# Optimization experiments

Hardware: AMD Instinct MI355X
Metric: run time of the kernel (lower is better)

## Reference

```python
import jax, jax.numpy as jnp
import numpy as np


def setup_inputs() -> dict:
    key = jax.random.key(0)
    k0, k1, k2, k3, k4 = jax.random.split(key, 5)
    B, S, H, I, E = 4, 2048, 1024, 3584, 8
    scale = 0.02
    return {
        "hidden_states": jax.random.normal(k0, (B, S, H), jnp.float32),
        "gate_w": jax.random.normal(k1, (E, H), jnp.float32) * scale,
        "Wg": jax.random.normal(k2, (E, I, H), jnp.float32) * scale,
        "Wu": jax.random.normal(k3, (E, I, H), jnp.float32) * scale,
        "Wd": jax.random.normal(k4, (E, H, I), jnp.float32) * scale,
        "top_k": 2,
    }


def reference(hidden_states, gate_w, Wg, Wu, Wd, top_k):
    B, S, H = hidden_states.shape
    E = gate_w.shape[0]
    x = hidden_states.reshape(-1, H)  # [N, H]

    # Router: softmax in float32 (matches torch dtype=torch.float), then top-k + renorm.
    router_logits = x @ gate_w.T  # [N, E]
    routing_probs = jax.nn.softmax(router_logits.astype(jnp.float32), axis=-1)
    top_w, sel = jax.lax.top_k(routing_probs, top_k)  # [N, K]
    top_w = top_w / jnp.sum(top_w, axis=-1, keepdims=True)
    top_w = top_w.astype(x.dtype)

    # Combined per-token weight for each expert: sum of top-k weights routed to it.
    # comb[n, e] = sum_k top_w[n, k] * (sel[n, k] == e)
    comb = jnp.einsum("nk,nke->ne", top_w, jax.nn.one_hot(sel, E, dtype=x.dtype))

    out = jnp.zeros_like(x)
    for e in range(E):  # fixed small loop over experts (structurally distinct weights)
        h = jax.nn.silu(x @ Wg[e].T) * (x @ Wu[e].T)  # [N, I] SwiGLU
        out = out + (h @ Wd[e].T) * comb[:, e:e + 1]
    return out.reshape(B, S, H), router_logits
```

## Files before the change

### kernel.cpp

```cpp
#include <hip/hip_runtime.h>
#include <hip/hip_bf16.h>

#define N_TOK 8192
#define H_DIM 1024
#define I_DIM 3584
#define N_EXP 8
#define N_PAIR (N_TOK * 2)

#define BM 256
#define BN 128
#define BK 32
#define MAX_TILES 72

#define NPAN1 (I_DIM / BN)
#define NPAN2 (H_DIM / BN)
#define NWG1  (MAX_TILES * NPAN1)
#define NWG2  (MAX_TILES * NPAN2)

typedef short bf16x8 __attribute__((ext_vector_type(8)));
typedef float f32x4 __attribute__((ext_vector_type(4)));

#define WS_CNT      0
#define WS_FILL     64
#define WS_OFF      128
#define WS_NTILES   192
#define WS_TILETAB  256
#define WS_SEL      2048
#define WS_WGT      (WS_SEL    + 2 * N_TOK * 4)
#define WS_PTOK     (WS_WGT    + 2 * N_TOK * 4)
#define WS_PW       (WS_PTOK   + N_PAIR * 4)
#define WS_XBF      (WS_PW     + N_PAIR * 4)
#define WS_HBUF     (WS_XBF    + (size_t)N_TOK * H_DIM * 2)
#define WBF_ELEMS   ((size_t)N_EXP * I_DIM * H_DIM)
#define WS_WGBF     (WS_HBUF + (size_t)N_PAIR * I_DIM * 2)
#define WS_WUBF     (WS_WGBF + WBF_ELEMS * 2)
#define WS_END      (WS_WUBF + WBF_ELEMS * 2)

__device__ __forceinline__ unsigned short f2bf(float f) {
  unsigned int u = __float_as_uint(f);
  unsigned int r = (u + 0x7fffu + ((u >> 16) & 1u)) >> 16;
  return (unsigned short)r;
}

__device__ __forceinline__ uint4 pack8(float4 a, float4 b) {
  uint4 r;
  r.x = (unsigned)f2bf(a.x) | ((unsigned)f2bf(a.y) << 16);
  r.y = (unsigned)f2bf(a.z) | ((unsigned)f2bf(a.w) << 16);
  r.z = (unsigned)f2bf(b.x) | ((unsigned)f2bf(b.y) << 16);
  r.w = (unsigned)f2bf(b.z) | ((unsigned)f2bf(b.w) << 16);
  return r;
}

__device__ __forceinline__ void gll16(const ushort* g, ushort* l) {
  __builtin_amdgcn_global_load_lds(
      (const __attribute__((address_space(1))) unsigned int*)g,
      (__attribute__((address_space(3))) unsigned int*)l, 16, 0, 0);
}

__global__ __launch_bounds__(64) void k_router(
    const float* __restrict__ x, const float* __restrict__ gw,
    float* __restrict__ logits, int* __restrict__ sel,
    float* __restrict__ wgt, int* __restrict__ cnt,
    ushort* __restrict__ xbf)
{
  const int n = blockIdx.x;
  const int lane = threadIdx.x;
  const float4* xr = (const float4*)(x + (size_t)n * H_DIM + lane * 16);
  float4 x0 = xr[0], x1 = xr[1], x2 = xr[2], x3 = xr[3];

  uint4* xo = (uint4*)(xbf + (size_t)n * H_DIM + lane * 16);
  xo[0] = pack8(x0, x1);
  xo[1] = pack8(x2, x3);

  float l[N_EXP];
#pragma unroll
  for (int e = 0; e < N_EXP; ++e) {
    const float4* wr = (const float4*)(gw + e * H_DIM + lane * 16);
    float4 w0 = wr[0], w1 = wr[1], w2 = wr[2], w3 = wr[3];
    float p = x0.x * w0.x + x0.y * w0.y + x0.z * w0.z + x0.w * w0.w
            + x1.x * w1.x + x1.y * w1.y + x1.z * w1.z + x1.w * w1.w
            + x2.x * w2.x + x2.y * w2.y + x2.z * w2.z + x2.w * w2.w
            + x3.x * w3.x + x3.y * w3.y + x3.z * w3.z + x3.w * w3.w;
#pragma unroll
    for (int o = 32; o >= 1; o >>= 1) p += __shfl_xor(p, o, 64);
    l[e] = p;
  }
  float m = l[0];
#pragma unroll
  for (int e = 1; e < N_EXP; ++e) m = fmaxf(m, l[e]);
  float pr[N_EXP]; float den = 0.f;
#pragma unroll
  for (int e = 0; e < N_EXP; ++e) { pr[e] = expf(l[e] - m); den += pr[e]; }
#pragma unroll
  for (int e = 0; e < N_EXP; ++e) pr[e] /= den;
  int i0 = 0; float p0 = pr[0];
#pragma unroll
  for (int e = 1; e < N_EXP; ++e) { if (pr[e] > p0) { p0 = pr[e]; i0 = e; } }
  int i1 = -1; float p1 = -1.f;
#pragma unroll
  for (int e = 0; e < N_EXP; ++e) { if (e != i0 && pr[e] > p1) { p1 = pr[e]; i1 = e; } }
  float rs = 1.f / (p0 + p1);
  if (lane == 0) {
    float* lo = logits + (size_t)n * N_EXP;
#pragma unroll
    for (int e = 0; e < N_EXP; ++e) lo[e] = l[e];
    sel[2 * n] = i0; sel[2 * n + 1] = i1;
    wgt[2 * n] = p0 * rs; wgt[2 * n + 1] = p1 * rs;
    atomicAdd(&cnt[i0], 1);
    atomicAdd(&cnt[i1], 1);
  }
}

__global__ void k_prefix(const int* __restrict__ cnt, int* __restrict__ off,
                         int* __restrict__ ntiles, int* __restrict__ tab)
{
  if (threadIdx.x != 0 || blockIdx.x != 0) return;
  int acc = 0, nt = 0;
  for (int e = 0; e < N_EXP; ++e) {
    off[e] = acc;
    int c = cnt[e];
    for (int r = 0; r < c; r += BM) {
      tab[nt * 3 + 0] = e;
      tab[nt * 3 + 1] = acc + r;
      tab[nt * 3 + 2] = (c - r < BM) ? (c - r) : BM;
      nt++;
    }
    acc += c;
  }
  off[N_EXP] = acc;
  *ntiles = nt;
}

__global__ __launch_bounds__(256) void k_scatter(
    const int* __restrict__ sel, const float* __restrict__ wgt,
    const int* __restrict__ off, int* __restrict__ fill,
    int* __restrict__ ptok, float* __restrict__ pw)
{
  int n = blockIdx.x * 256 + threadIdx.x;
  if (n >= N_TOK) return;
#pragma unroll
  for (int k = 0; k < 2; ++k) {
    int e = sel[2 * n + k];
    int pos = atomicAdd(&fill[e], 1);
    int row = off[e] + pos;
    ptok[row] = n;
    pw[row] = wgt[2 * n + k];
  }
}

__global__ __launch_bounds__(256) void k_cvtw(const float* __restrict__ src,
                                              ushort* __restrict__ dst)
{
  size_t i = (size_t)blockIdx.x * 256 + threadIdx.x;
  const float4* s = (const float4*)(src + i * 8);
  float4 a = s[0], b = s[1];
  ((uint4*)dst)[i] = pack8(a, b);
}


__global__ __launch_bounds__(512) void k_mlp1b(
    const ushort* __restrict__ Wg, const ushort* __restrict__ Wu,
    const ushort* __restrict__ xbf, const int* __restrict__ ptok,
    const int* __restrict__ ntiles, const int* __restrict__ tab,
    ushort* __restrict__ hbuf)
{
  __shared__ ushort sA[2][BM * BK];
  __shared__ ushort sG[2][BN * BK];
  __shared__ ushort sU[2][BN * BK];
  __shared__ int stok[BM];

  const int orig = blockIdx.x;
  const int lin = (orig & 7) * (NWG1 >> 3) + (orig >> 3);
  const int tile = lin / NPAN1;
  const int i0 = (lin % NPAN1) * BN;

  if (tile >= *ntiles) return;
  const int e = tab[tile * 3 + 0];
  const int row0 = tab[tile * 3 + 1];
  const int nrows = tab[tile * 3 + 2];
  const int t = threadIdx.x;

  if (t < BM) {
    int tt = t < nrows ? t : (nrows - 1);
    stok[t] = ptok[row0 + tt];
  }
  __syncthreads();

  const int ak = (t & 3) * 8;
  const int ar = t >> 2;
  const ushort* ga0 = xbf + (size_t)stok[ar] * H_DIM + ak;
  const ushort* ga1 = xbf + (size_t)stok[128 + ar] * H_DIM + ak;

  const ushort* gg0 = Wg + (size_t)e * I_DIM * H_DIM + (size_t)(i0 + ar) * H_DIM + ak;
  const ushort* gu0 = Wu + (size_t)e * I_DIM * H_DIM + (size_t)(i0 + ar) * H_DIM + ak;

  const int lane = t & 63, wid = t >> 6;
  const int wm = wid >> 1, wn = wid & 1;
  const int fr = lane & 15, fq = lane >> 4;

  f32x4 ag[4][4], au[4][4];
#pragma unroll
  for (int m = 0; m < 4; ++m)
#pragma unroll
    for (int n = 0; n < 4; ++n) { ag[m][n] = (f32x4){0,0,0,0}; au[m][n] = (f32x4){0,0,0,0}; }

#define STAGE1(b, kt) do {                      \
    gll16(ga0 + (kt), &sA[b][t * 8]);           \
    gll16(ga1 + (kt), &sA[b][(512 + t) * 8]);   \
    gll16(gg0 + (kt), &sG[b][t * 8]);           \
    gll16(gu0 + (kt), &sU[b][t * 8]);           \
  } while (0)

#define COMPUTE1(b) do {                                                     \
    bf16x8 a[4], bg[4], bu[4];                                               \
    _Pragma("unroll")                                                        \
    for (int m = 0; m < 4; ++m)                                              \
      a[m] = *(const bf16x8*)(&sA[b][(wm * 64 + m * 16 + fr) * BK + fq * 8]);\
    _Pragma("unroll")                                                        \
    for (int n = 0; n < 4; ++n) {                                            \
      bg[n] = *(const bf16x8*)(&sG[b][(wn * 64 + n * 16 + fr) * BK + fq * 8]);\
      bu[n] = *(const bf16x8*)(&sU[b][(wn * 64 + n * 16 + fr) * BK + fq * 8]);\
    }                                                                        \
    _Pragma("unroll")                                                        \
    for (int m = 0; m < 4; ++m)                                              \
      _Pragma("unroll")                                                      \
      for (int n = 0; n < 4; ++n) {                                          \
        ag[m][n] = __builtin_amdgcn_mfma_f32_16x16x32_bf16(a[m], bg[n], ag[m][n], 0, 0, 0); \
        au[m][n] = __builtin_amdgcn_mfma_f32_16x16x32_bf16(a[m], bu[n], au[m][n], 0, 0, 0); \
      }                                                                      \
  } while (0)

  const int NK = H_DIM / BK;
  STAGE1(0, 0);
  __syncthreads();
  for (int ki = 0; ki < NK - 1; ++ki) {
    const int cur = ki & 1;
    STAGE1(cur ^ 1, (ki + 1) * BK);
    COMPUTE1(cur);
    __syncthreads();
  }
  COMPUTE1((NK - 1) & 1);
#undef STAGE1
#undef COMPUTE1

#pragma unroll
  for (int m = 0; m < 4; ++m) {
    const int rb = wm * 64 + m * 16 + fq * 4;
#pragma unroll
    for (int n = 0; n < 4; ++n) {
      const int col = i0 + wn * 64 + n * 16 + fr;
#pragma unroll
      for (int r = 0; r < 4; ++r) {
        const int row = rb + r;
        if (row < nrows) {
          float g = ag[m][n][r], u = au[m][n][r];
          float hv = (g / (1.f + __expf(-g))) * u;
          hbuf[(size_t)(row0 + row) * I_DIM + col] = f2bf(hv);
        }
      }
    }
  }
}

__global__ __launch_bounds__(512) void k_mlp2b(
    const ushort* __restrict__ Wd, const ushort* __restrict__ hbuf,
    const int* __restrict__ ptok, const float* __restrict__ pw,
    const int* __restrict__ ntiles, const int* __restrict__ tab,
    float* __restrict__ out)
{
  __shared__ ushort sA[2][BM * BK];
  __shared__ ushort sB[2][BN * BK];
  __shared__ int stok[BM];
  __shared__ float sw[BM];

  const int orig = blockIdx.x;
  const int lin = (orig & 7) * (NWG2 >> 3) + (orig >> 3);
  const int tile = lin / NPAN2;
  const int j0 = (lin % NPAN2) * BN;

  if (tile >= *ntiles) return;
  const int e = tab[tile * 3 + 0];
  const int row0 = tab[tile * 3 + 1];
  const int nrows = tab[tile * 3 + 2];
  const int t = threadIdx.x;

  if (t < BM) {
    int tt = t < nrows ? t : (nrows - 1);
    stok[t] = ptok[row0 + tt];
    sw[t] = pw[row0 + tt];
  }
  __syncthreads();

  const int ak = (t & 3) * 8;
  const int ar = t >> 2;
  int arow0 = row0 + ar;        if (arow0 > N_PAIR - 1) arow0 = N_PAIR - 1;
  int arow1 = row0 + 128 + ar;  if (arow1 > N_PAIR - 1) arow1 = N_PAIR - 1;
  const ushort* ga0 = hbuf + (size_t)arow0 * I_DIM + ak;
  const ushort* ga1 = hbuf + (size_t)arow1 * I_DIM + ak;

  const ushort* gb0 = Wd + (size_t)e * H_DIM * I_DIM + (size_t)(j0 + ar) * I_DIM + ak;

  const int lane = t & 63, wid = t >> 6;
  const int wm = wid >> 1, wn = wid & 1;
  const int fr = lane & 15, fq = lane >> 4;

  f32x4 ac[4][4];
#pragma unroll
  for (int m = 0; m < 4; ++m)
#pragma unroll
    for (int n = 0; n < 4; ++n) ac[m][n] = (f32x4){0,0,0,0};

#define STAGE2(b, kt) do {                      \
    gll16(ga0 + (kt), &sA[b][t * 8]);           \
    gll16(ga1 + (kt), &sA[b][(512 + t) * 8]);   \
    gll16(gb0 + (kt), &sB[b][t * 8]);           \
  } while (0)

#define COMPUTE2(b) do {                                                     \
    bf16x8 a[4], bb[4];                                                      \
    _Pragma("unroll")                                                        \
    for (int m = 0; m < 4; ++m)                                              \
      a[m] = *(const bf16x8*)(&sA[b][(wm * 64 + m * 16 + fr) * BK + fq * 8]);\
    _Pragma("unroll")                                                        \
    for (int n = 0; n < 4; ++n)                                              \
      bb[n] = *(const bf16x8*)(&sB[b][(wn * 64 + n * 16 + fr) * BK + fq * 8]);\
    _Pragma("unroll")                                                        \
    for (int m = 0; m < 4; ++m)                                              \
      _Pragma("unroll")                                                      \
      for (int n = 0; n < 4; ++n)                                            \
        ac[m][n] = __builtin_amdgcn_mfma_f32_16x16x32_bf16(a[m], bb[n], ac[m][n], 0, 0, 0); \
  } while (0)

  const int NK = I_DIM / BK;
  STAGE2(0, 0);
  __syncthreads();
  for (int ki = 0; ki < NK - 1; ++ki) {
    const int cur = ki & 1;
    STAGE2(cur ^ 1, (ki + 1) * BK);
    COMPUTE2(cur);
    __syncthreads();
  }
  COMPUTE2((NK - 1) & 1);
#undef STAGE2
#undef COMPUTE2

#pragma unroll
  for (int m = 0; m < 4; ++m) {
    const int rb = wm * 64 + m * 16 + fq * 4;
#pragma unroll
    for (int n = 0; n < 4; ++n) {
      const int col = j0 + wn * 64 + n * 16 + fr;
#pragma unroll
      for (int r = 0; r < 4; ++r) {
        const int row = rb + r;
        if (row < nrows) {
          float v = ac[m][n][r] * sw[row];
          atomicAdd(&out[(size_t)stok[row] * H_DIM + col], v);
        }
      }
    }
  }
}


#define FBM 128

__global__ __launch_bounds__(256) void k_mlp1(
    const float* __restrict__ Wg, const float* __restrict__ Wu,
    const ushort* __restrict__ xbf, const int* __restrict__ ptok,
    const int* __restrict__ ntiles, const int* __restrict__ tab,
    ushort* __restrict__ hbuf)
{
  __shared__ ushort sA[FBM * BK];
  __shared__ ushort sG[BN * BK];
  __shared__ ushort sU[BN * BK];
  __shared__ int stok[FBM];

  const int tile = blockIdx.x;
  if (tile >= *ntiles) return;
  const int e = tab[tile * 3 + 0];
  const int row0 = tab[tile * 3 + 1] + (blockIdx.z ? FBM : 0);
  int nrows = tab[tile * 3 + 2] - (blockIdx.z ? FBM : 0);
  if (nrows <= 0) return;
  if (nrows > FBM) nrows = FBM;
  const int i0 = blockIdx.y * BN;
  const int t = threadIdx.x;

  if (t < FBM) {
    int tt = t < nrows ? t : (nrows - 1);
    stok[t] = ptok[row0 + tt];
  }
  __syncthreads();

  const int ak = (t & 3) * 8;
  const ushort* ga0 = xbf + (size_t)stok[t >> 2] * H_DIM + ak;
  const ushort* ga1 = xbf + (size_t)stok[64 + (t >> 2)] * H_DIM + ak;
  ushort* la0 = sA + (size_t)t * 8;
  ushort* la1 = sA + (size_t)(256 + t) * 8;

  const int wr = t >> 1, wcb = (t & 1) * 16;
  const float* gwg = Wg + (size_t)e * I_DIM * H_DIM + (size_t)(i0 + wr) * H_DIM + wcb;
  const float* gwu = Wu + (size_t)e * I_DIM * H_DIM + (size_t)(i0 + wr) * H_DIM + wcb;
  ushort* lwg = sG + wr * BK + wcb;
  ushort* lwu = sU + wr * BK + wcb;

  const int lane = t & 63, wid = t >> 6;
  const int wm = wid >> 1, wn = wid & 1;
  const int fr = lane & 15, fq = lane >> 4;

  f32x4 ag[4][4], au[4][4];
#pragma unroll
  for (int m = 0; m < 4; ++m)
#pragma unroll
    for (int n = 0; n < 4; ++n) { ag[m][n] = (f32x4){0,0,0,0}; au[m][n] = (f32x4){0,0,0,0}; }

  for (int kt = 0; kt < H_DIM; kt += BK) {
    gll16(ga0 + kt, la0);
    gll16(ga1 + kt, la1);

    const float4* pg = (const float4*)(gwg + kt);
    const float4* pu = (const float4*)(gwu + kt);
    float4 g0 = pg[0], g1 = pg[1], g2 = pg[2], g3 = pg[3];
    float4 u0 = pu[0], u1 = pu[1], u2 = pu[2], u3 = pu[3];
    ((uint4*)lwg)[0] = pack8(g0, g1);
    ((uint4*)lwg)[1] = pack8(g2, g3);
    ((uint4*)lwu)[0] = pack8(u0, u1);
    ((uint4*)lwu)[1] = pack8(u2, u3);
    __syncthreads();

    bf16x8 a[4], bg[4], bu[4];
#pragma unroll
    for (int m = 0; m < 4; ++m)
      a[m] = *(const bf16x8*)(sA + (wm * 64 + m * 16 + fr) * BK + fq * 8);
#pragma unroll
    for (int n = 0; n < 4; ++n) {
      bg[n] = *(const bf16x8*)(sG + (wn * 64 + n * 16 + fr) * BK + fq * 8);
      bu[n] = *(const bf16x8*)(sU + (wn * 64 + n * 16 + fr) * BK + fq * 8);
    }
#pragma unroll
    for (int m = 0; m < 4; ++m)
#pragma unroll
      for (int n = 0; n < 4; ++n) {
        ag[m][n] = __builtin_amdgcn_mfma_f32_16x16x32_bf16(a[m], bg[n], ag[m][n], 0, 0, 0);
        au[m][n] = __builtin_amdgcn_mfma_f32_16x16x32_bf16(a[m], bu[n], au[m][n], 0, 0, 0);
      }
    __syncthreads();
  }

#pragma unroll
  for (int m = 0; m < 4; ++m) {
    const int rb = wm * 64 + m * 16 + fq * 4;
#pragma unroll
    for (int n = 0; n < 4; ++n) {
      const int col = i0 + wn * 64 + n * 16 + fr;
#pragma unroll
      for (int r = 0; r < 4; ++r) {
        const int row = rb + r;
        if (row < nrows) {
          float g = ag[m][n][r], u = au[m][n][r];
          float hv = (g / (1.f + __expf(-g))) * u;
          hbuf[(size_t)(row0 + row) * I_DIM + col] = f2bf(hv);
        }
      }
    }
  }
}

__global__ __launch_bounds__(256) void k_mlp2(
    const float* __restrict__ Wd, const ushort* __restrict__ hbuf,
    const int* __restrict__ ptok, const float* __restrict__ pw,
    const int* __restrict__ ntiles, const int* __restrict__ tab,
    float* __restrict__ out)
{
  __shared__ ushort sA[FBM * BK];
  __shared__ ushort sB[BN * BK];
  __shared__ int stok[FBM];
  __shared__ float sw[FBM];

  const int tile = blockIdx.x;
  if (tile >= *ntiles) return;
  const int e = tab[tile * 3 + 0];
  const int row0 = tab[tile * 3 + 1] + (blockIdx.z ? FBM : 0);
  int nrows = tab[tile * 3 + 2] - (blockIdx.z ? FBM : 0);
  if (nrows <= 0) return;
  if (nrows > FBM) nrows = FBM;
  const int j0 = blockIdx.y * BN;
  const int t = threadIdx.x;

  if (t < FBM) {
    int tt = t < nrows ? t : (nrows - 1);
    stok[t] = ptok[row0 + tt];
    sw[t] = pw[row0 + tt];
  }
  __syncthreads();

  const int ak = (t & 3) * 8;
  int arow0 = row0 + (t >> 2);       if (arow0 > N_PAIR - 1) arow0 = N_PAIR - 1;
  int arow1 = row0 + 64 + (t >> 2);  if (arow1 > N_PAIR - 1) arow1 = N_PAIR - 1;
  const ushort* ga0 = hbuf + (size_t)arow0 * I_DIM + ak;
  const ushort* ga1 = hbuf + (size_t)arow1 * I_DIM + ak;
  ushort* la0 = sA + (size_t)t * 8;
  ushort* la1 = sA + (size_t)(256 + t) * 8;

  const int wr = t >> 1, wcb = (t & 1) * 16;
  const float* gb = Wd + (size_t)e * H_DIM * I_DIM + (size_t)(j0 + wr) * I_DIM + wcb;
  ushort* lb = sB + wr * BK + wcb;

  const int lane = t & 63, wid = t >> 6;
  const int wm = wid >> 1, wn = wid & 1;
  const int fr = lane & 15, fq = lane >> 4;

  f32x4 ac[4][4];
#pragma unroll
  for (int m = 0; m < 4; ++m)
#pragma unroll
    for (int n = 0; n < 4; ++n) ac[m][n] = (f32x4){0,0,0,0};

  for (int kt = 0; kt < I_DIM; kt += BK) {
    gll16(ga0 + kt, la0);
    gll16(ga1 + kt, la1);

    const float4* pb = (const float4*)(gb + kt);
    float4 b0 = pb[0], b1 = pb[1], b2 = pb[2], b3 = pb[3];
    ((uint4*)lb)[0] = pack8(b0, b1);
    ((uint4*)lb)[1] = pack8(b2, b3);
    __syncthreads();

    bf16x8 a[4], bb[4];
#pragma unroll
    for (int m = 0; m < 4; ++m)
      a[m] = *(const bf16x8*)(sA + (wm * 64 + m * 16 + fr) * BK + fq * 8);
#pragma unroll
    for (int n = 0; n < 4; ++n)
      bb[n] = *(const bf16x8*)(sB + (wn * 64 + n * 16 + fr) * BK + fq * 8);
#pragma unroll
    for (int m = 0; m < 4; ++m)
#pragma unroll
      for (int n = 0; n < 4; ++n)
        ac[m][n] = __builtin_amdgcn_mfma_f32_16x16x32_bf16(a[m], bb[n], ac[m][n], 0, 0, 0);
    __syncthreads();
  }

#pragma unroll
  for (int m = 0; m < 4; ++m) {
    const int rb = wm * 64 + m * 16 + fq * 4;
#pragma unroll
    for (int n = 0; n < 4; ++n) {
      const int col = j0 + wn * 64 + n * 16 + fr;
#pragma unroll
      for (int r = 0; r < 4; ++r) {
        const int row = rb + r;
        if (row < nrows) {
          float v = ac[m][n][r] * sw[row];
          atomicAdd(&out[(size_t)stok[row] * H_DIM + col], v);
        }
      }
    }
  }
}

extern "C" void kernel_launch(void* const* d_in, const int* in_sizes, int n_in,
                              void* d_out, int out_size, void* d_ws, size_t ws_size,
                              hipStream_t stream)
{
  const float* x  = (const float*)d_in[0];
  const float* gw = (const float*)d_in[1];
  const float* Wg = (const float*)d_in[2];
  const float* Wu = (const float*)d_in[3];
  const float* Wd = (const float*)d_in[4];

  float* out    = (float*)d_out;
  float* logits = out + (size_t)N_TOK * H_DIM;

  char* ws = (char*)d_ws;
  int*    cnt    = (int*)(ws + WS_CNT);
  int*    fill   = (int*)(ws + WS_FILL);
  int*    off    = (int*)(ws + WS_OFF);
  int*    ntiles = (int*)(ws + WS_NTILES);
  int*    tab    = (int*)(ws + WS_TILETAB);
  int*    sel    = (int*)(ws + WS_SEL);
  float*  wgt    = (float*)(ws + WS_WGT);
  int*    ptok   = (int*)(ws + WS_PTOK);
  float*  pw     = (float*)(ws + WS_PW);
  ushort* xbf    = (ushort*)(ws + WS_XBF);
  ushort* hbuf   = (ushort*)(ws + WS_HBUF);
  ushort* wgbf   = (ushort*)(ws + WS_WGBF);
  ushort* wubf   = (ushort*)(ws + WS_WUBF);
  ushort* wdbf   = wgbf;

  const bool fast = (ws_size >= WS_END);

  hipMemsetAsync(d_out, 0, (size_t)N_TOK * H_DIM * sizeof(float), stream);
  hipMemsetAsync(ws, 0, 128, stream);

  k_router<<<N_TOK, 64, 0, stream>>>(x, gw, logits, sel, wgt, cnt, xbf);
  k_prefix<<<1, 64, 0, stream>>>(cnt, off, ntiles, tab);
  k_scatter<<<N_TOK / 256, 256, 0, stream>>>(sel, wgt, off, fill, ptok, pw);

  const int cvtblocks = (int)(WBF_ELEMS / 8 / 256);

  if (fast) {
    k_cvtw<<<cvtblocks, 256, 0, stream>>>(Wg, wgbf);
    k_cvtw<<<cvtblocks, 256, 0, stream>>>(Wu, wubf);
    k_mlp1b<<<NWG1, 512, 0, stream>>>(wgbf, wubf, xbf, ptok, ntiles, tab, hbuf);
    k_cvtw<<<cvtblocks, 256, 0, stream>>>(Wd, wdbf);
    k_mlp2b<<<NWG2, 512, 0, stream>>>(wdbf, hbuf, ptok, pw, ntiles, tab, out);
  } else {
    dim3 gA(MAX_TILES, I_DIM / BN, 2);
    dim3 gB(MAX_TILES, H_DIM / BN, 2);
    k_mlp1<<<gA, 256, 0, stream>>>(Wg, Wu, xbf, ptok, ntiles, tab, hbuf);
    k_mlp2<<<gB, 256, 0, stream>>>(Wd, hbuf, ptok, pw, ntiles, tab, out);
  }
}
```

Baseline: 985.1 us.

## Overlap global-to-LDS staging with MFMA via manual waitcnt and barriers

Restructures both expert GEMM main loops into a two-stage prefetch pipeline. The next-next tile is issued right after compute, and the loop waits with partial vmcnt counts and raw s_barrier instead of __syncthreads. The goal is to keep global loads in flight while the MFMAs run, instead of draining all memory traffic at each barrier. The hard-coded vmcnt values assume a fixed number of load instructions per STAGE macro (4 and 3), so a different code generation could cause races.

```diff
diff --git a/kernel.cpp b/kernel.cpp
--- a/kernel.cpp
+++ b/kernel.cpp
@@ -19,6 +19,8 @@
 
 typedef short bf16x8 __attribute__((ext_vector_type(8)));
 typedef float f32x4 __attribute__((ext_vector_type(4)));
+
+#define CFENCE() asm volatile("" ::: "memory")
 
 #define WS_CNT      0
 #define WS_FILL     64
@@ -232,14 +234,33 @@
 
   const int NK = H_DIM / BK;
   STAGE1(0, 0);
-  __syncthreads();
-  for (int ki = 0; ki < NK - 1; ++ki) {
+  CFENCE();
+  STAGE1(1, BK);
+#pragma unroll 2
+  for (int ki = 0; ki < NK - 2; ++ki) {
     const int cur = ki & 1;
-    STAGE1(cur ^ 1, (ki + 1) * BK);
+    asm volatile("s_waitcnt vmcnt(4)" ::: "memory");
+    __builtin_amdgcn_s_barrier();
+    CFENCE();
+    __builtin_amdgcn_sched_barrier(0);
     COMPUTE1(cur);
-    __syncthreads();
-  }
-  COMPUTE1((NK - 1) & 1);
+    asm volatile("s_waitcnt lgkmcnt(0)" ::: "memory");
+    __builtin_amdgcn_sched_barrier(0);
+    __builtin_amdgcn_s_barrier();
+    CFENCE();
+    STAGE1(cur, (ki + 2) * BK);
+  }
+  asm volatile("s_waitcnt vmcnt(4)" ::: "memory");
+  __builtin_amdgcn_s_barrier();
+  CFENCE();
+  __builtin_amdgcn_sched_barrier(0);
+  COMPUTE1(0);
+  CFENCE();
+  asm volatile("s_waitcnt vmcnt(0) lgkmcnt(0)" ::: "memory");
+  __builtin_amdgcn_s_barrier();
+  CFENCE();
+  __builtin_amdgcn_sched_barrier(0);
+  COMPUTE1(1);
 #undef STAGE1
 #undef COMPUTE1
 
@@ -333,14 +354,33 @@
 
   const int NK = I_DIM / BK;
   STAGE2(0, 0);
-  __syncthreads();
-  for (int ki = 0; ki < NK - 1; ++ki) {
+  CFENCE();
+  STAGE2(1, BK);
+#pragma unroll 2
+  for (int ki = 0; ki < NK - 2; ++ki) {
     const int cur = ki & 1;
-    STAGE2(cur ^ 1, (ki + 1) * BK);
+    asm volatile("s_waitcnt vmcnt(3)" ::: "memory");
+    __builtin_amdgcn_s_barrier();
+    CFENCE();
+    __builtin_amdgcn_sched_barrier(0);
     COMPUTE2(cur);
-    __syncthreads();
-  }
-  COMPUTE2((NK - 1) & 1);
+    asm volatile("s_waitcnt lgkmcnt(0)" ::: "memory");
+    __builtin_amdgcn_sched_barrier(0);
+    __builtin_amdgcn_s_barrier();
+    CFENCE();
+    STAGE2(cur, (ki + 2) * BK);
+  }
+  asm volatile("s_waitcnt vmcnt(3)" ::: "memory");
+  __builtin_amdgcn_s_barrier();
+  CFENCE();
+  __builtin_amdgcn_sched_barrier(0);
+  COMPUTE2(0);
+  CFENCE();
+  asm volatile("s_waitcnt vmcnt(0) lgkmcnt(0)" ::: "memory");
+  __builtin_amdgcn_s_barrier();
+  CFENCE();
+  __builtin_amdgcn_sched_barrier(0);
+  COMPUTE2(1);
 #undef STAGE2
 #undef COMPUTE2
 
```

Result: no change. 980.1 us (-0.5%).
